# Kernel tuning notes

Hardware: AMD Instinct MI355X
Metric: run time of the kernel (lower is better)

## Reference

```python
import jax, jax.numpy as jnp
import numpy as np

T, B, D, H = 256, 128, 512, 512  # seq_len, batch, input_dim, hidden_dim (= n_qubits)


def setup_inputs() -> dict:
    key = jax.random.key(0)
    ks = jax.random.split(key, 17)
    s = 0.02
    inp = {"inputs": jax.random.normal(ks[0], (T, B, D), dtype=jnp.float32)}
    for j, n in enumerate(["f", "i", "u", "o"]):
        inp["W" + n] = jax.random.normal(ks[1 + 4 * j], (D + H, H), dtype=jnp.float32) * s
        inp["b" + n] = jnp.zeros((H,), jnp.float32)
        inp["rx" + n] = jax.random.normal(ks[2 + 4 * j], (H,), dtype=jnp.float32)
        inp["P" + n] = jax.random.normal(ks[3 + 4 * j], (H, H), dtype=jnp.float32) * s
    return inp


def _qlayer(z, rx, P):
    # per-wire trainable rotation RX(theta) acting on the scalar feature of each
    # wire (scales it by cos(theta)), followed by the bias-free `pre` linear.
    return (z * jnp.cos(rx)) @ P


def reference(inputs, Wf, bf, Wi, bi, Wu, bu, Wo, bo, rxf, rxi, rxu, rxo, Pf, Pi, Pu, Po):
    Bc, Hc = inputs.shape[1], bf.shape[0]

    def step(carry, x_t):
        hx, cx = carry
        comb = jnp.concatenate([x_t, hx], axis=1)  # (B, D+H)
        f = jax.nn.sigmoid(_qlayer(comb @ Wf + bf, rxf, Pf))
        i = jax.nn.sigmoid(_qlayer(comb @ Wi + bi, rxi, Pi))
        g = jnp.tanh(_qlayer(comb @ Wu + bu, rxu, Pu))
        o = jax.nn.sigmoid(_qlayer(comb @ Wo + bo, rxo, Po))
        cx = f * cx + i * g
        hx = o * jnp.tanh(cx)
        return (hx, cx), hx

    h0 = jnp.zeros((Bc, Hc), inputs.dtype)
    (hx, cx), outputs = jax.lax.scan(step, (h0, h0), inputs)
    return outputs, hx, cx
```

## Files before the change

kernel.cpp:

```cpp
#include <hip/hip_runtime.h>
#include <hip/hip_bf16.h>

typedef __attribute__((ext_vector_type(8))) short bf16x8;
typedef __attribute__((ext_vector_type(4))) float f32x4;
typedef unsigned short u16;
typedef unsigned int u32;

__device__ __forceinline__ u16 f2bf(float f) {
  union { float f; unsigned u; } v; v.f = f;
  unsigned r = v.u + 0x7FFFu + ((v.u >> 16) & 1u);
  return (u16)(r >> 16);
}

__device__ __forceinline__ float sigm_fast(float x) {
  return __builtin_amdgcn_rcpf(1.f + __expf(-x));
}
__device__ __forceinline__ float tanh_fast(float x) {
  x = fminf(fmaxf(x, -15.f), 15.f);
  float e = __expf(2.f * x);
  return (e - 1.f) * __builtin_amdgcn_rcpf(e + 1.f);
}

__device__ __forceinline__ void ld_llc_b128(const u16* p, bf16x8& r) {
  asm volatile("global_load_dwordx4 %0, %1, off sc0 sc1" : "=&v"(r) : "v"(p));
}
__device__ __forceinline__ void ld_g_b128(const u16* p, bf16x8& r) {
  asm volatile("global_load_dwordx4 %0, %1, off" : "=&v"(r) : "v"(p));
}
__device__ __forceinline__ void st_llc_b32(u32* p, u32 v) {
  asm volatile("global_store_dword %0, %1, off sc0 sc1" :: "v"(p), "v"(v) : "memory");
}
__device__ __forceinline__ void st_g_b32(u32* p, u32 v) {
  asm volatile("global_store_dword %0, %1, off" :: "v"(p), "v"(v) : "memory");
}

__global__ __launch_bounds__(256) void fold_kernel(
    const float* __restrict__ W0, const float* __restrict__ rx0, const float* __restrict__ P0,
    const float* __restrict__ W1, const float* __restrict__ rx1, const float* __restrict__ P1,
    const float* __restrict__ W2, const float* __restrict__ rx2, const float* __restrict__ P2,
    const float* __restrict__ W3, const float* __restrict__ rx3, const float* __restrict__ P3,
    u16* __restrict__ Wt)
{
  const int g = blockIdx.z;
  const float* W  = (g == 0) ? W0  : (g == 1) ? W1  : (g == 2) ? W2  : W3;
  const float* rx = (g == 0) ? rx0 : (g == 1) ? rx1 : (g == 2) ? rx2 : rx3;
  const float* P  = (g == 0) ? P0  : (g == 1) ? P1  : (g == 2) ? P2  : P3;
  __shared__ __align__(16) float As[16][68];
  __shared__ __align__(16) float Bs[16][68];
  const int bk = blockIdx.x, bj = blockIdx.y;
  const int tid = threadIdx.x;
  const int tx = tid & 15, ty = tid >> 4;
  const int j0 = bj * 64, k0 = bk * 64;
  float acc[4][4] = {};
  for (int m0 = 0; m0 < 512; m0 += 16) {
#pragma unroll
    for (int l = 0; l < 4; ++l) {
      int lin = tid + 256 * l;
      int mm = lin >> 6, jr = lin & 63;
      As[mm][jr] = P[(m0 + mm) * 512 + j0 + jr];
      int kk = lin >> 4, mb = lin & 15;
      Bs[mb][kk] = W[(k0 + kk) * 512 + m0 + mb] * cosf(rx[m0 + mb]);
    }
    __syncthreads();
#pragma unroll
    for (int mm = 0; mm < 16; ++mm) {
      f32x4 a = *(const f32x4*)&As[mm][ty * 4];
      f32x4 b = *(const f32x4*)&Bs[mm][tx * 4];
#pragma unroll
      for (int i = 0; i < 4; ++i)
#pragma unroll
        for (int jj = 0; jj < 4; ++jj)
          acc[i][jj] += a[i] * b[jj];
    }
    __syncthreads();
  }
#pragma unroll
  for (int i = 0; i < 4; ++i) {
    int j = j0 + ty * 4 + i;
    size_t n = (size_t)(j * 4 + g);
    ushort4 w;
    w.x = f2bf(acc[i][0]); w.y = f2bf(acc[i][1]);
    w.z = f2bf(acc[i][2]); w.w = f2bf(acc[i][3]);
    *(ushort4*)(Wt + n * 1024 + k0 + tx * 4) = w;
  }
}

__global__ __launch_bounds__(256) void fold_bias(
    const float* __restrict__ b0, const float* __restrict__ rx0, const float* __restrict__ P0,
    const float* __restrict__ b1, const float* __restrict__ rx1, const float* __restrict__ P1,
    const float* __restrict__ b2, const float* __restrict__ rx2, const float* __restrict__ P2,
    const float* __restrict__ b3, const float* __restrict__ rx3, const float* __restrict__ P3,
    float* __restrict__ bpn)
{
  const int g = blockIdx.x >> 3, jb = blockIdx.x & 7;
  const float* b  = (g == 0) ? b0  : (g == 1) ? b1  : (g == 2) ? b2  : b3;
  const float* rx = (g == 0) ? rx0 : (g == 1) ? rx1 : (g == 2) ? rx2 : rx3;
  const float* P  = (g == 0) ? P0  : (g == 1) ? P1  : (g == 2) ? P2  : P3;
  __shared__ float bc[512];
  __shared__ float red[4][65];
  const int tid = threadIdx.x;
  bc[tid] = b[tid] * cosf(rx[tid]);
  bc[tid + 256] = b[tid + 256] * cosf(rx[tid + 256]);
  __syncthreads();
  const int jl = tid & 63, msub = tid >> 6;
  const int j = jb * 64 + jl;
  float acc = 0.f;
  for (int m = msub * 128; m < msub * 128 + 128; ++m)
    acc += bc[m] * P[m * 512 + j];
  red[msub][jl] = acc;
  __syncthreads();
  if (msub == 0)
    bpn[j * 4 + g] = red[0][jl] + red[1][jl] + red[2][jl] + red[3][jl];
}

__global__ __launch_bounds__(256) void xcvt_kernel(
    const float* __restrict__ x, u16* __restrict__ xb)
{
  size_t i = (size_t)blockIdx.x * 256 + threadIdx.x;
  f32x4 v = *(const f32x4*)(x + i * 4);
  ushort4 w;
  w.x = f2bf(v[0]); w.y = f2bf(v[1]); w.z = f2bf(v[2]); w.w = f2bf(v[3]);
  *(ushort4*)(xb + i * 4) = w;
}

__global__ __launch_bounds__(256) void init_kernel(unsigned* hbuf32, float* cbuf,
                                                   unsigned* flags) {
  int i = blockIdx.x * 256 + threadIdx.x;
  hbuf32[i] = 0;
  cbuf[i] = 0.f;
  if (i < 256) flags[i] = 0;
}

__global__ __launch_bounds__(256) void tail_kernel(
    const float* __restrict__ hlast, const float* __restrict__ c,
    float* __restrict__ hx, float* __restrict__ cx)
{
  int i = blockIdx.x * 256 + threadIdx.x;
  hx[i] = hlast[i];
  cx[i] = c[i];
}

__global__ __launch_bounds__(256) void step_kernel(
    const u16* __restrict__ xb_t, const u16* __restrict__ h_in,
    u16* __restrict__ h_out, const u16* __restrict__ Wt,
    const float* __restrict__ bpn, float* __restrict__ cbuf,
    float* __restrict__ out_t)
{
  __shared__ float pre_s[32][33];
  const int bid = blockIdx.x;
  const int mb = bid >> 6, nb = bid & 63;
  const int b0 = mb * 32, n0 = nb * 32;
  const int tid = threadIdx.x;
  const int wv = tid >> 6, lane = tid & 63;
  const int rt = wv >> 1, nt = wv & 1;
  const int l15 = lane & 15, kg = lane >> 4;
  const int brow = b0 + rt * 16 + l15;
  const int ncol = n0 + nt * 16 + l15;
  const u16* wrow = Wt + (size_t)ncol * 1024;
  const u16* xrow = xb_t + (size_t)brow * 512;
  const u16* hrow = h_in + (size_t)brow * 512;
  f32x4 acc = {0.f, 0.f, 0.f, 0.f};
#pragma unroll 8
  for (int kk = 0; kk < 32; ++kk) {
    const int kb = kk * 32 + kg * 8;
    bf16x8 bfrag = *(const bf16x8*)(wrow + kb);
    bf16x8 afrag;
    if (kb < 512) afrag = *(const bf16x8*)(xrow + kb);
    else          afrag = *(const bf16x8*)(hrow + (kb - 512));
    acc = __builtin_amdgcn_mfma_f32_16x16x32_bf16(afrag, bfrag, acc, 0, 0, 0);
  }
  const float bias = bpn[ncol];
#pragma unroll
  for (int q = 0; q < 4; ++q)
    pre_s[rt * 16 + kg * 4 + q][nt * 16 + l15] = acc[q] + bias;
  __syncthreads();
  const int bb = tid >> 3, jo = tid & 7;
  float pf = pre_s[bb][jo * 4 + 0];
  float pi = pre_s[bb][jo * 4 + 1];
  float pu = pre_s[bb][jo * 4 + 2];
  float po = pre_s[bb][jo * 4 + 3];
  float fg = 1.f / (1.f + __expf(-pf));
  float ig = 1.f / (1.f + __expf(-pi));
  float gg = tanhf(pu);
  float og = 1.f / (1.f + __expf(-po));
  size_t idx = (size_t)(b0 + bb) * 512 + (size_t)(nb * 8 + jo);
  float cv = fg * cbuf[idx] + ig * gg;
  cbuf[idx] = cv;
  float hv = og * tanhf(cv);
  out_t[idx] = hv;
  h_out[idx] = f2bf(hv);
}

__global__ __launch_bounds__(256, 1) void qlstm_persistent(
    const u16* __restrict__ Xbf,
    u16* __restrict__ hbuf,
    const u16* __restrict__ Wt,
    const float* __restrict__ bpn,
    float* __restrict__ out,
    unsigned* __restrict__ flags)
{
  __shared__ float pre_s[32][33];
  const int bid = blockIdx.x;
  const int mb = bid >> 6, nb = bid & 63;
  const int b0 = mb * 32, n0 = nb * 32;
  const int tid = threadIdx.x;
  const int wv = tid >> 6, lane = tid & 63;
  const int rt = wv >> 1, nt = wv & 1;
  const int l15 = lane & 15, kg = lane >> 4;
  const int brow = b0 + rt * 16 + l15;
  const int ncol = n0 + nt * 16 + l15;

  const u16* wrow = Wt + (size_t)ncol * 1024;
  bf16x8 warr[32];
#pragma unroll
  for (int kk = 0; kk < 32; ++kk)
    warr[kk] = *(const bf16x8*)(wrow + kk * 32 + kg * 8);
  const float bnc = bpn[ncol];

  const int bb = tid >> 3, jo = tid & 7;
  const size_t eidx = (size_t)(b0 + bb) * 512 + (size_t)(nb * 8 + jo);
  float cst = 0.f, hl = 0.f;

  bf16x8 xf[16];
  {
    const u16* xr = Xbf + (size_t)brow * 512;
#pragma unroll
    for (int kk = 0; kk < 16; ++kk)
      ld_g_b128(xr + kk * 32 + kg * 8, xf[kk]);
    asm volatile("s_waitcnt vmcnt(0)" ::: "memory");
  }

  for (int t = 0; t < 256; ++t) {
    if (t > 0 && tid < 64) {
      int guard = 0;
      while (__hip_atomic_load(&flags[mb * 64 + tid], __ATOMIC_RELAXED,
                               __HIP_MEMORY_SCOPE_AGENT) < (unsigned)t) {
        if (++guard > 2000000) break;
      }
    }
    __builtin_amdgcn_s_barrier();
    asm volatile("" ::: "memory");

    bf16x8 hf[16];
    if (t > 0) {
      const u16* hr = hbuf + (size_t)((t & 1) ? 65536 : 0) + (size_t)brow * 512;
#pragma unroll
      for (int kk = 0; kk < 16; ++kk)
        ld_llc_b128(hr + kk * 32 + kg * 8, hf[kk]);
    }

    asm volatile("s_waitcnt vmcnt(16)" ::: "memory");
    __builtin_amdgcn_sched_barrier(0);
    f32x4 ax0 = {0,0,0,0}, ax1 = {0,0,0,0};
#pragma unroll
    for (int kk = 0; kk < 16; kk += 2) {
      ax0 = __builtin_amdgcn_mfma_f32_16x16x32_bf16(xf[kk],     warr[kk],     ax0, 0, 0, 0);
      ax1 = __builtin_amdgcn_mfma_f32_16x16x32_bf16(xf[kk + 1], warr[kk + 1], ax1, 0, 0, 0);
    }

    f32x4 ah0 = {0,0,0,0}, ah1 = {0,0,0,0};
    if (t > 0) {
      asm volatile("s_waitcnt vmcnt(0)" ::: "memory");
      __builtin_amdgcn_sched_barrier(0);
#pragma unroll
      for (int kk = 0; kk < 16; kk += 2) {
        ah0 = __builtin_amdgcn_mfma_f32_16x16x32_bf16(hf[kk],     warr[16 + kk],     ah0, 0, 0, 0);
        ah1 = __builtin_amdgcn_mfma_f32_16x16x32_bf16(hf[kk + 1], warr[16 + kk + 1], ah1, 0, 0, 0);
      }
    }
    f32x4 acc = (ax0 + ax1) + (ah0 + ah1);

#pragma unroll
    for (int q = 0; q < 4; ++q)
      pre_s[rt * 16 + kg * 4 + q][nt * 16 + l15] = acc[q] + bnc;
    asm volatile("s_waitcnt lgkmcnt(0)" ::: "memory");
    __builtin_amdgcn_sched_barrier(0);
    __builtin_amdgcn_s_barrier();
    asm volatile("" ::: "memory");

    float pf = pre_s[bb][jo * 4 + 0];
    float pi = pre_s[bb][jo * 4 + 1];
    float pu = pre_s[bb][jo * 4 + 2];
    float po = pre_s[bb][jo * 4 + 3];
    cst = sigm_fast(pf) * cst + sigm_fast(pi) * tanh_fast(pu);
    float hv = sigm_fast(po) * tanh_fast(cst);
    hl = hv;

    u16 myh = f2bf(hv);
    u32 partner = (u32)(u16)__shfl_xor((int)(u32)myh, 1);
    u16* hnext = hbuf + (size_t)(((t + 1) & 1) ? 65536 : 0);
    if ((tid & 1) == 0)
      st_llc_b32((u32*)(hnext + eidx), (u32)myh | (partner << 16));
    asm volatile("s_waitcnt vmcnt(0)" ::: "memory");
    __builtin_amdgcn_s_barrier();
    asm volatile("" ::: "memory");
    if (tid == 0)
      (void)__hip_atomic_exchange(&flags[bid], (unsigned)(t + 1),
                                  __ATOMIC_RELAXED, __HIP_MEMORY_SCOPE_AGENT);

    union { float f; u32 u; } ho; ho.f = hv;
    st_g_b32((u32*)(out + (size_t)t * 65536 + eidx), ho.u);
    if (t < 255) {
      const u16* xr = Xbf + (size_t)(t + 1) * 65536 + (size_t)brow * 512;
#pragma unroll
      for (int kk = 0; kk < 16; ++kk)
        ld_g_b128(xr + kk * 32 + kg * 8, xf[kk]);
    }
  }

  asm volatile("s_waitcnt vmcnt(0)" ::: "memory");
  out[(size_t)256 * 65536 + eidx] = hl;
  out[(size_t)256 * 65536 + 65536 + eidx] = cst;
}

extern "C" void kernel_launch(void* const* d_in, const int* in_sizes, int n_in,
                              void* d_out, int out_size, void* d_ws, size_t ws_size,
                              hipStream_t stream) {
  (void)in_sizes; (void)n_in; (void)out_size; (void)ws_size;
  const float* inp = (const float*)d_in[0];
  float* out = (float*)d_out;

  char* base = (char*)d_ws;
  u16*      Xbf   = (u16*)base;
  u16*      Wt    = (u16*)(base + 33554432);
  float*    bpn   = (float*)(base + 33554432 + 4194304);
  u16*      hbuf  = (u16*)(base + 33554432 + 4194304 + 8192);
  unsigned* flags = (unsigned*)(base + 33554432 + 4194304 + 8192 + 262144);
  float*    cbuf  = (float*)(base + 33554432 + 4194304 + 8192 + 262144 + 1024);

  const float* W[4];  const float* b[4];  const float* rx[4];  const float* P[4];
  for (int g = 0; g < 4; ++g) {
    W[g]  = (const float*)d_in[1 + 4 * g];
    b[g]  = (const float*)d_in[2 + 4 * g];
    rx[g] = (const float*)d_in[3 + 4 * g];
    P[g]  = (const float*)d_in[4 + 4 * g];
  }
  fold_kernel<<<dim3(16, 8, 4), 256, 0, stream>>>(
      W[0], rx[0], P[0], W[1], rx[1], P[1],
      W[2], rx[2], P[2], W[3], rx[3], P[3], Wt);
  fold_bias<<<dim3(32), 256, 0, stream>>>(
      b[0], rx[0], P[0], b[1], rx[1], P[1],
      b[2], rx[2], P[2], b[3], rx[3], P[3], bpn);
  xcvt_kernel<<<16384, 256, 0, stream>>>(inp, Xbf);
  init_kernel<<<256, 256, 0, stream>>>((unsigned*)hbuf, cbuf, flags);

  void* args[6];
  const u16* Xbf_c = Xbf;
  const u16* Wt_c = Wt;
  const float* bpn_c = bpn;
  u16* hbuf_p = hbuf;
  float* out_p = out;
  unsigned* flags_p = flags;
  args[0] = (void*)&Xbf_c;
  args[1] = (void*)&hbuf_p;
  args[2] = (void*)&Wt_c;
  args[3] = (void*)&bpn_c;
  args[4] = (void*)&out_p;
  args[5] = (void*)&flags_p;
  hipError_t e = hipLaunchCooperativeKernel((const void*)qlstm_persistent,
                                            dim3(256), dim3(256), args, 0, stream);
  if (e != hipSuccess) {
    for (int t = 0; t < 256; ++t) {
      const u16* xb_t  = Xbf + (size_t)t * 65536;
      const u16* h_in  = hbuf + (size_t)(t & 1) * 65536;
      u16*       h_oup = hbuf + (size_t)((t & 1) ^ 1) * 65536;
      float*     out_t = out + (size_t)t * 65536;
      step_kernel<<<256, 256, 0, stream>>>(xb_t, h_in, h_oup, Wt, bpn, cbuf, out_t);
    }
    tail_kernel<<<256, 256, 0, stream>>>(out + (size_t)255 * 65536, cbuf,
                                         out + (size_t)256 * 65536,
                                         out + (size_t)256 * 65536 + 65536);
  }
}
```

Measured before the change: 1.395 ms.

## Make each wave independent with per-wave flags, removing block barriers in recurrent loop

Re-tiles the persistent LSTM so each block handles 16 batch rows by 64 gate columns, and each wave owns a 16x16 tile whose gate outputs it finishes itself through wave-private LDS. This removes all block-level barriers from the time loop. Synchronisation becomes per wave: each wave publishes its own flag and spins on only the two producer flags it needs, using a wave vote. Hidden-state stores become 64-bit writes. The change cuts barrier and flag latency on the serial critical path, in exchange for more flags to poll and more redundant x/h loads per block.

New measurement: 2.295 ms. 64.5% more time.

```diff
diff --git a/kernel.cpp b/kernel.cpp
--- a/kernel.cpp
+++ b/kernel.cpp
@@ -3,6 +3,7 @@
 
 typedef __attribute__((ext_vector_type(8))) short bf16x8;
 typedef __attribute__((ext_vector_type(4))) float f32x4;
+typedef __attribute__((ext_vector_type(2))) unsigned int u32x2;
 typedef unsigned short u16;
 typedef unsigned int u32;
 
@@ -27,8 +28,8 @@
 __device__ __forceinline__ void ld_g_b128(const u16* p, bf16x8& r) {
   asm volatile("global_load_dwordx4 %0, %1, off" : "=&v"(r) : "v"(p));
 }
-__device__ __forceinline__ void st_llc_b32(u32* p, u32 v) {
-  asm volatile("global_store_dword %0, %1, off sc0 sc1" :: "v"(p), "v"(v) : "memory");
+__device__ __forceinline__ void st_llc_b64(u16* p, u32x2 v) {
+  asm volatile("global_store_dwordx2 %0, %1, off sc0 sc1" :: "v"(p), "v"(v) : "memory");
 }
 __device__ __forceinline__ void st_g_b32(u32* p, u32 v) {
   asm volatile("global_store_dword %0, %1, off" :: "v"(p), "v"(v) : "memory");
@@ -123,12 +124,12 @@
   *(ushort4*)(xb + i * 4) = w;
 }
 
-__global__ __launch_bounds__(256) void init_kernel(unsigned* hbuf32, float* cbuf,
-                                                   unsigned* flags) {
+__global__ __launch_bounds__(256) void init_kernel(u32* hbuf32, float* cbuf,
+                                                   u32* flags) {
   int i = blockIdx.x * 256 + threadIdx.x;
   hbuf32[i] = 0;
   cbuf[i] = 0.f;
-  if (i < 256) flags[i] = 0;
+  if (i < 1024) flags[i] = 0;
 }
 
 __global__ __launch_bounds__(256) void tail_kernel(
@@ -197,18 +198,18 @@
     const u16* __restrict__ Wt,
     const float* __restrict__ bpn,
     float* __restrict__ out,
-    unsigned* __restrict__ flags)
-{
-  __shared__ float pre_s[32][33];
+    u32* __restrict__ flags)
+{
+  __shared__ float pre_s[4][16][17];
   const int bid = blockIdx.x;
-  const int mb = bid >> 6, nb = bid & 63;
-  const int b0 = mb * 32, n0 = nb * 32;
+  const int g  = bid & 7;
+  const int nb = bid >> 3;
+  const int b0 = g * 16;
   const int tid = threadIdx.x;
   const int wv = tid >> 6, lane = tid & 63;
-  const int rt = wv >> 1, nt = wv & 1;
   const int l15 = lane & 15, kg = lane >> 4;
-  const int brow = b0 + rt * 16 + l15;
-  const int ncol = n0 + nt * 16 + l15;
+  const int brow = b0 + l15;
+  const int ncol = nb * 64 + wv * 16 + l15;
 
   const u16* wrow = Wt + (size_t)ncol * 1024;
   bf16x8 warr[32];
@@ -217,8 +218,11 @@
     warr[kk] = *(const bf16x8*)(wrow + kk * 32 + kg * 8);
   const float bnc = bpn[ncol];
 
-  const int bb = tid >> 3, jo = tid & 7;
-  const size_t eidx = (size_t)(b0 + bb) * 512 + (size_t)(nb * 8 + jo);
+  const int jglob = nb * 16 + wv * 4 + kg;
+  const size_t eidx = (size_t)brow * 512 + (size_t)jglob;
+  const size_t hrow_off = (size_t)brow * 512 + (size_t)(nb * 16 + wv * 4);
+  const int fi1 = 4 * g + 32 * (lane >> 2) + (lane & 3);
+  const int fi2 = fi1 + 512;
   float cst = 0.f, hl = 0.f;
 
   bf16x8 xf[16];
@@ -231,15 +235,18 @@
   }
 
   for (int t = 0; t < 256; ++t) {
-    if (t > 0 && tid < 64) {
+    if (t > 0) {
       int guard = 0;
-      while (__hip_atomic_load(&flags[mb * 64 + tid], __ATOMIC_RELAXED,
-                               __HIP_MEMORY_SCOPE_AGENT) < (unsigned)t) {
+      for (;;) {
+        u32 f1 = __hip_atomic_load(&flags[fi1], __ATOMIC_RELAXED,
+                                   __HIP_MEMORY_SCOPE_AGENT);
+        u32 f2 = __hip_atomic_load(&flags[fi2], __ATOMIC_RELAXED,
+                                   __HIP_MEMORY_SCOPE_AGENT);
+        if (__all((int)(f1 >= (u32)t && f2 >= (u32)t))) break;
         if (++guard > 2000000) break;
       }
-    }
-    __builtin_amdgcn_s_barrier();
-    asm volatile("" ::: "memory");
+      asm volatile("" ::: "memory");
+    }
 
     bf16x8 hf[16];
     if (t > 0) {
@@ -249,8 +256,6 @@
         ld_llc_b128(hr + kk * 32 + kg * 8, hf[kk]);
     }
 
-    asm volatile("s_waitcnt vmcnt(16)" ::: "memory");
-    __builtin_amdgcn_sched_barrier(0);
     f32x4 ax0 = {0,0,0,0}, ax1 = {0,0,0,0};
 #pragma unroll
     for (int kk = 0; kk < 16; kk += 2) {
@@ -272,30 +277,29 @@
 
 #pragma unroll
     for (int q = 0; q < 4; ++q)
-      pre_s[rt * 16 + kg * 4 + q][nt * 16 + l15] = acc[q] + bnc;
+      pre_s[wv][kg * 4 + q][l15] = acc[q] + bnc;
     asm volatile("s_waitcnt lgkmcnt(0)" ::: "memory");
     __builtin_amdgcn_sched_barrier(0);
-    __builtin_amdgcn_s_barrier();
-    asm volatile("" ::: "memory");
-
-    float pf = pre_s[bb][jo * 4 + 0];
-    float pi = pre_s[bb][jo * 4 + 1];
-    float pu = pre_s[bb][jo * 4 + 2];
-    float po = pre_s[bb][jo * 4 + 3];
-    cst = sigm_fast(pf) * cst + sigm_fast(pi) * tanh_fast(pu);
-    float hv = sigm_fast(po) * tanh_fast(cst);
+    f32x4 g4 = *(const f32x4*)&pre_s[wv][l15][kg * 4];
+    asm volatile("s_waitcnt lgkmcnt(0)" ::: "memory");
+    __builtin_amdgcn_sched_barrier(0);
+
+    cst = sigm_fast(g4[0]) * cst + sigm_fast(g4[1]) * tanh_fast(g4[2]);
+    float hv = sigm_fast(g4[3]) * tanh_fast(cst);
     hl = hv;
 
     u16 myh = f2bf(hv);
-    u32 partner = (u32)(u16)__shfl_xor((int)(u32)myh, 1);
+    u32 w  = (u32)myh | ((u32)(u16)__shfl_xor((int)(u32)myh, 16) << 16);
+    u32 w2 = (u32)__shfl_xor((int)w, 32);
     u16* hnext = hbuf + (size_t)(((t + 1) & 1) ? 65536 : 0);
-    if ((tid & 1) == 0)
-      st_llc_b32((u32*)(hnext + eidx), (u32)myh | (partner << 16));
+    if (kg == 0) {
+      u32x2 hw = {w, w2};
+      st_llc_b64(hnext + hrow_off, hw);
+    }
     asm volatile("s_waitcnt vmcnt(0)" ::: "memory");
-    __builtin_amdgcn_s_barrier();
-    asm volatile("" ::: "memory");
-    if (tid == 0)
-      (void)__hip_atomic_exchange(&flags[bid], (unsigned)(t + 1),
+
+    if (lane == 0)
+      (void)__hip_atomic_exchange(&flags[bid * 4 + wv], (u32)(t + 1),
                                   __ATOMIC_RELAXED, __HIP_MEMORY_SCOPE_AGENT);
 
     union { float f; u32 u; } ho; ho.f = hv;
@@ -321,12 +325,12 @@
   float* out = (float*)d_out;
 
   char* base = (char*)d_ws;
-  u16*      Xbf   = (u16*)base;
-  u16*      Wt    = (u16*)(base + 33554432);
-  float*    bpn   = (float*)(base + 33554432 + 4194304);
-  u16*      hbuf  = (u16*)(base + 33554432 + 4194304 + 8192);
-  unsigned* flags = (unsigned*)(base + 33554432 + 4194304 + 8192 + 262144);
-  float*    cbuf  = (float*)(base + 33554432 + 4194304 + 8192 + 262144 + 1024);
+  u16*   Xbf   = (u16*)base;
+  u16*   Wt    = (u16*)(base + 33554432);
+  float* bpn   = (float*)(base + 33554432 + 4194304);
+  u16*   hbuf  = (u16*)(base + 33554432 + 4194304 + 8192);
+  u32*   flags = (u32*)(base + 33554432 + 4194304 + 8192 + 262144);
+  float* cbuf  = (float*)(base + 33554432 + 4194304 + 8192 + 262144 + 4096);
 
   const float* W[4];  const float* b[4];  const float* rx[4];  const float* P[4];
   for (int g = 0; g < 4; ++g) {
@@ -342,7 +346,7 @@
       b[0], rx[0], P[0], b[1], rx[1], P[1],
       b[2], rx[2], P[2], b[3], rx[3], P[3], bpn);
   xcvt_kernel<<<16384, 256, 0, stream>>>(inp, Xbf);
-  init_kernel<<<256, 256, 0, stream>>>((unsigned*)hbuf, cbuf, flags);
+  init_kernel<<<256, 256, 0, stream>>>((u32*)hbuf, cbuf, flags);
 
   void* args[6];
   const u16* Xbf_c = Xbf;
@@ -350,7 +354,7 @@
   const float* bpn_c = bpn;
   u16* hbuf_p = hbuf;
   float* out_p = out;
-  unsigned* flags_p = flags;
+  u32* flags_p = flags;
   args[0] = (void*)&Xbf_c;
   args[1] = (void*)&hbuf_p;
   args[2] = (void*)&Wt_c;
```
